# Performance work log

Measured on AMD Instinct MI355X. Metric: run time of the kernel, lower is better.

## Reference

```python
import jax, jax.numpy as jnp
import numpy as np

COMMITMENT = 0.25  # beta


def setup_inputs() -> dict:
    key = jax.random.key(0)
    k1, k2 = jax.random.split(key)
    B, M, D, K = 16, 4096, 64, 1024
    z_e = jax.random.normal(k1, (B, M, D), dtype=jnp.float32)
    embed = jax.random.normal(k2, (K, D), dtype=jnp.float32)  # codebook C in R^{KxD}
    return {"z_e": z_e, "embed": embed}


def reference(z_e, embed):
    """Eval-mode VQ forward: nearest-code lookup + VQ loss + straight-through.

    z_e:   (B, M, D) encoder outputs
    embed: (K, D) codebook
    Returns (z_q_st, indices, vq_loss).
    """
    B, M, D = z_e.shape
    flat = z_e.reshape(-1, D)  # (N, D)
    dist = (
        jnp.sum(flat * flat, axis=1, keepdims=True)
        - 2.0 * (flat @ embed.T)
        + jnp.sum(embed * embed, axis=1)[None, :]
    )
    indices = jnp.argmin(dist, axis=1)  # (N,)
    z_q = embed[indices].reshape(B, M, D)  # gather

    sg = jax.lax.stop_gradient
    codebook_loss = jnp.mean((z_q - sg(z_e)) ** 2)
    commitment_loss = jnp.mean((z_e - sg(z_q)) ** 2)
    vq_loss = codebook_loss + COMMITMENT * commitment_loss

    z_q_st = z_e + sg(z_q - z_e)  # straight-through estimator
    return z_q_st, indices.reshape(B, M), vq_loss
```

## Files before the change

kernel.cpp:

```cpp
#include <hip/hip_runtime.h>
#include <hip/hip_bf16.h>
#include <stdint.h>

#define D_     64
#define K_     1024
#define N_     65536
#define TPB    256
#define RPB    64
#define NBLK   (N_ / RPB)
#define MARGIN 0.06f

typedef __bf16 bf16x8 __attribute__((ext_vector_type(8)));
typedef float  f32x4  __attribute__((ext_vector_type(4)));

__device__ __forceinline__ unsigned short bf16_rne(float f) {
    union { float f; uint32_t u; } v; v.f = f;
    const uint32_t u = v.u;
    return (unsigned short)((u + 0x7fffu + ((u >> 16) & 1u)) >> 16);
}
__device__ __forceinline__ float bf16_tof(unsigned short h) {
    union { uint32_t u; float f; } v; v.u = ((uint32_t)h) << 16;
    return v.f;
}

__global__ __launch_bounds__(256) void vq_prep(const float* __restrict__ embed,
                                               double* __restrict__ n64,
                                               float* __restrict__ n32,
                                               char* __restrict__ eb) {
    const int gid = blockIdx.x * 256 + threadIdx.x;
    const int k   = gid >> 2;
    const int q4  = gid & 3;
    const float4* e4 = (const float4*)(embed + (size_t)k * D_ + q4 * 16);
    double acc = 0.0;
    uint32_t hw[8], lw[8];
#pragma unroll
    for (int q = 0; q < 4; ++q) {
        const float4 e = e4[q];
        float c[4] = {e.x, e.y, e.z, e.w};
        unsigned short hb[4], lb[4];
#pragma unroll
        for (int j = 0; j < 4; ++j) {
            hb[j] = bf16_rne(c[j]);
            lb[j] = bf16_rne(c[j] - bf16_tof(hb[j]));
            acc = fma((double)c[j], (double)c[j], acc);
        }
        hw[q * 2]     = (uint32_t)hb[0] | ((uint32_t)hb[1] << 16);
        hw[q * 2 + 1] = (uint32_t)hb[2] | ((uint32_t)hb[3] << 16);
        lw[q * 2]     = (uint32_t)lb[0] | ((uint32_t)lb[1] << 16);
        lw[q * 2 + 1] = (uint32_t)lb[2] | ((uint32_t)lb[3] << 16);
    }
    acc += __shfl_xor(acc, 1);
    acc += __shfl_xor(acc, 2);
    if (q4 == 0) { n64[k] = acc; n32[k] = (float)acc; }
    const int ct = k >> 4, cl = k & 15;
    char* hp = eb + (size_t)ct * 4096        + (q4 * 16 + cl) * 32;
    char* lp = eb + (size_t)ct * 4096 + 2048 + (q4 * 16 + cl) * 32;
    int4 h0; h0.x = hw[0]; h0.y = hw[1]; h0.z = hw[2]; h0.w = hw[3];
    int4 h1; h1.x = hw[4]; h1.y = hw[5]; h1.z = hw[6]; h1.w = hw[7];
    int4 l0; l0.x = lw[0]; l0.y = lw[1]; l0.z = lw[2]; l0.w = lw[3];
    int4 l1; l1.x = lw[4]; l1.y = lw[5]; l1.z = lw[6]; l1.w = lw[7];
    *(int4*)hp = h0; *(int4*)(hp + 16) = h1;
    *(int4*)lp = l0; *(int4*)(lp + 16) = l1;
}

__global__ __launch_bounds__(TPB) void vq_main(const float* __restrict__ z_e,
                                               const float* __restrict__ embed,
                                               const char* __restrict__ eb,
                                               const float* __restrict__ n32g,
                                               const double* __restrict__ n64g,
                                               float* __restrict__ out,
                                               float* __restrict__ partials) {
    __shared__ float red[TPB];

    const int tid  = threadIdx.x;
    const int lane = tid & 63;
    const int w    = tid >> 6;
    const int lg   = lane >> 4;
    const int lc   = lane & 15;
    const int wrow0 = blockIdx.x * RPB + w * 16;

    float  xs[16];
    bf16x8 ah[2], al[2];
    {
        const int row = wrow0 + lc;
        const float4* xg = (const float4*)(z_e + (size_t)row * D_ + lg * 16);
#pragma unroll
        for (int q = 0; q < 4; ++q) {
            const float4 x = xg[q];
            xs[q * 4 + 0] = x.x; xs[q * 4 + 1] = x.y;
            xs[q * 4 + 2] = x.z; xs[q * 4 + 3] = x.w;
        }
#pragma unroll
        for (int s = 0; s < 2; ++s) {
#pragma unroll
            for (int i = 0; i < 8; ++i) {
                const float xf = xs[s * 8 + i];
                const unsigned short hb = bf16_rne(xf);
                const unsigned short lb = bf16_rne(xf - bf16_tof(hb));
                union { unsigned short u; __bf16 h; } uh, ul;
                uh.u = hb; ul.u = lb;
                ah[s][i] = uh.h;
                al[s][i] = ul.h;
            }
        }
    }

    float b1[4], b2[4];
    int   i1[4];
#pragma unroll
    for (int rg = 0; rg < 4; ++rg) { b1[rg] = 3.4e38f; b2[rg] = 3.4e38f; i1[rg] = 0; }

    const char* ebl = eb + lane * 32;

#define LOADCT(CT, H0, H1, L0, L1, NV) {                                  \
        const char* p_ = ebl + (CT) * 4096;                               \
        H0 = *(const int4*)(p_);                                          \
        H1 = *(const int4*)(p_ + 16);                                     \
        L0 = *(const int4*)(p_ + 2048);                                   \
        L1 = *(const int4*)(p_ + 2064);                                   \
        NV = n32g[(CT) * 16 + lc];                                        \
    }
#define COMPUTECT(CT, H0, H1, L0, L1, NV) {                               \
        const bf16x8 bh0 = __builtin_bit_cast(bf16x8, H0);                \
        const bf16x8 bh1 = __builtin_bit_cast(bf16x8, H1);                \
        const bf16x8 bl0 = __builtin_bit_cast(bf16x8, L0);                \
        const bf16x8 bl1 = __builtin_bit_cast(bf16x8, L1);                \
        f32x4 acc0 = {0.f, 0.f, 0.f, 0.f};                                \
        f32x4 acc1 = {0.f, 0.f, 0.f, 0.f};                                \
        acc0 = __builtin_amdgcn_mfma_f32_16x16x32_bf16(ah[0], bh0, acc0, 0, 0, 0); \
        acc1 = __builtin_amdgcn_mfma_f32_16x16x32_bf16(ah[1], bh1, acc1, 0, 0, 0); \
        acc0 = __builtin_amdgcn_mfma_f32_16x16x32_bf16(al[0], bh0, acc0, 0, 0, 0); \
        acc1 = __builtin_amdgcn_mfma_f32_16x16x32_bf16(al[1], bh1, acc1, 0, 0, 0); \
        acc0 = __builtin_amdgcn_mfma_f32_16x16x32_bf16(ah[0], bl0, acc0, 0, 0, 0); \
        acc1 = __builtin_amdgcn_mfma_f32_16x16x32_bf16(ah[1], bl1, acc1, 0, 0, 0); \
        const int ki = (CT) * 16 + lc;                                    \
        _Pragma("unroll")                                                 \
        for (int rg = 0; rg < 4; ++rg) {                                  \
            const float s  = fmaf(-2.0f, acc0[rg] + acc1[rg], NV);        \
            const bool  lt = s < b1[rg];                                  \
            const float m2 = fminf(s, b2[rg]);                            \
            b2[rg] = lt ? b1[rg] : m2;                                    \
            b1[rg] = lt ? s      : b1[rg];                                \
            i1[rg] = lt ? ki     : i1[rg];                                \
        }                                                                 \
    }

    {
        int4 Ah0, Ah1, Al0, Al1; float Anv;
        int4 Bh0, Bh1, Bl0, Bl1; float Bnv;
        LOADCT(0, Ah0, Ah1, Al0, Al1, Anv);
        for (int ct = 0; ct < 64; ct += 2) {
            LOADCT(ct + 1, Bh0, Bh1, Bl0, Bl1, Bnv);
            COMPUTECT(ct, Ah0, Ah1, Al0, Al1, Anv);
            const int nct = (ct + 2 < 64) ? (ct + 2) : 0;
            LOADCT(nct, Ah0, Ah1, Al0, Al1, Anv);
            COMPUTECT(ct + 1, Bh0, Bh1, Bl0, Bl1, Bnv);
        }
    }
#undef LOADCT
#undef COMPUTECT

#pragma unroll
    for (int rg = 0; rg < 4; ++rg)
#pragma unroll
        for (int off = 1; off <= 8; off <<= 1) {
            const float ob1 = __shfl_xor(b1[rg], off);
            const float ob2 = __shfl_xor(b2[rg], off);
            const int   oi1 = __shfl_xor(i1[rg], off);
            if (ob1 < b1[rg] || (ob1 == b1[rg] && oi1 < i1[rg])) {
                b2[rg] = fminf(b1[rg], ob2); b1[rg] = ob1; i1[rg] = oi1;
            } else {
                b2[rg] = fminf(ob1, b2[rg]);
            }
        }

#pragma unroll
    for (int rg = 0; rg < 4; ++rg) {
        for (int g = 0; g < 4; ++g) {
            const float g1 = __shfl(b1[rg], g << 4);
            const float g2 = __shfl(b2[rg], g << 4);
            if (g2 - g1 < MARGIN) {
                const int grow = wrow0 + g * 4 + rg;
                const float* xp = z_e + (size_t)grow * D_;
                double bs = 1.0e300; int bi = 1 << 30;
                for (int c0 = 0; c0 < K_; c0 += 64) {
                    const int c = c0 + lane;
                    const float* ep = embed + (size_t)c * D_;
                    double dot = 0.0;
#pragma unroll
                    for (int j = 0; j < D_; ++j)
                        dot = fma((double)xp[j], (double)ep[j], dot);
                    const double sc = fma(-2.0, dot, n64g[c]);
                    if (sc < bs) { bs = sc; bi = c; }
                }
#pragma unroll
                for (int off = 32; off > 0; off >>= 1) {
                    const double so = __shfl_xor(bs, off);
                    const int    io = __shfl_xor(bi, off);
                    if (so < bs || (so == bs && io < bi)) { bs = so; bi = io; }
                }
                if (lg == g) i1[rg] = bi;
            }
        }
    }

    float sq = 0.f;
    {
        const int srcl = (lc >> 2) << 4;
        const int c0v = __shfl(i1[0], srcl);
        const int c1v = __shfl(i1[1], srcl);
        const int c2v = __shfl(i1[2], srcl);
        const int c3v = __shfl(i1[3], srcl);
        const int rsel = lc & 3;
        int bidx = (rsel == 0) ? c0v : (rsel == 1) ? c1v : (rsel == 2) ? c2v : c3v;
        bidx &= (K_ - 1);
        const int row = wrow0 + lc;
        const float4* eg = (const float4*)(embed + (size_t)bidx * D_ + lg * 16);
        float4*       og = (float4*)(out + (size_t)row * D_ + lg * 16);
#pragma unroll
        for (int q = 0; q < 4; ++q) {
            const float4 e = eg[q];
            const int   x0 = q * 4;
            const float d0 = e.x - xs[x0 + 0];
            const float d1 = e.y - xs[x0 + 1];
            const float d2 = e.z - xs[x0 + 2];
            const float d3 = e.w - xs[x0 + 3];
            sq = fmaf(d0, d0, sq); sq = fmaf(d1, d1, sq);
            sq = fmaf(d2, d2, sq); sq = fmaf(d3, d3, sq);
            float4 o;
            o.x = xs[x0 + 0] + d0;
            o.y = xs[x0 + 1] + d1;
            o.z = xs[x0 + 2] + d2;
            o.w = xs[x0 + 3] + d3;
            og[q] = o;
        }
        if (lg == 0) out[(size_t)N_ * D_ + row] = (float)bidx;
    }

    red[tid] = sq;
    __syncthreads();
#pragma unroll
    for (int s = TPB / 2; s > 0; s >>= 1) {
        if (tid < s) red[tid] += red[tid + s];
        __syncthreads();
    }
    if (tid == 0) partials[blockIdx.x] = red[0];
}

__global__ __launch_bounds__(256) void vq_loss_final(const float* __restrict__ partials,
                                                     float* __restrict__ out) {
    __shared__ float red[256];
    const int tid = threadIdx.x;
    float s = 0.f;
#pragma unroll
    for (int i = 0; i < NBLK / 256; ++i) s += partials[tid + i * 256];
    red[tid] = s;
    __syncthreads();
#pragma unroll
    for (int w = 128; w > 0; w >>= 1) {
        if (tid < w) red[tid] += red[tid + w];
        __syncthreads();
    }
    if (tid == 0)
        out[(size_t)N_ * D_ + N_] = 1.25f * red[0] / (float)((size_t)N_ * D_);
}

extern "C" void kernel_launch(void* const* d_in, const int* in_sizes, int n_in,
                              void* d_out, int out_size, void* d_ws, size_t ws_size,
                              hipStream_t stream) {
    const float* z_e;
    const float* embed;
    if (in_sizes[0] == N_ * D_) {
        z_e   = (const float*)d_in[0];
        embed = (const float*)d_in[1];
    } else {
        z_e   = (const float*)d_in[1];
        embed = (const float*)d_in[0];
    }
    float* out = (float*)d_out;

    double* n64      = (double*)d_ws;
    float*  n32      = (float*)(n64 + K_);
    float*  partials = n32 + K_;
    char*   eb       = (char*)(partials + NBLK);

    vq_prep<<<(K_ * 4) / 256, 256, 0, stream>>>(embed, n64, n32, eb);
    vq_main<<<NBLK, TPB, 0, stream>>>(z_e, embed, eb, n32, n64, out, partials);
    vq_loss_final<<<1, 256, 0, stream>>>(partials, out);
}
```

Measured before the change: 204.6 us.

## Use single-wave blocks, deeper codebook prefetch, and re-read inputs instead of holding registers

The main kernel now runs one 64-thread wave per block covering 16 rows, which removes the shared-memory block reduction and its barriers in favour of a wave shuffle reduction. The codebook loop loads two 16-code tiles per step with double buffering, deepening the prefetch. The fp32 input row is no longer kept in registers across the loop; it is re-read from global memory in the epilogue to lower register pressure. The prep kernel splits its double accumulation into two chains. In exchange there are four times as many blocks, vq_loss_final has more partials to sum, and the extra input read adds memory traffic.

```diff
diff --git a/kernel.cpp b/kernel.cpp
--- a/kernel.cpp
+++ b/kernel.cpp
@@ -5,8 +5,8 @@
 #define D_     64
 #define K_     1024
 #define N_     65536
-#define TPB    256
-#define RPB    64
+#define TPB    64
+#define RPB    16
 #define NBLK   (N_ / RPB)
 #define MARGIN 0.06f
 
@@ -23,15 +23,15 @@
     return v.f;
 }
 
-__global__ __launch_bounds__(256) void vq_prep(const float* __restrict__ embed,
-                                               double* __restrict__ n64,
-                                               float* __restrict__ n32,
-                                               char* __restrict__ eb) {
-    const int gid = blockIdx.x * 256 + threadIdx.x;
+__global__ __launch_bounds__(64) void vq_prep(const float* __restrict__ embed,
+                                              double* __restrict__ n64,
+                                              float* __restrict__ n32,
+                                              char* __restrict__ eb) {
+    const int gid = blockIdx.x * 64 + threadIdx.x;
     const int k   = gid >> 2;
     const int q4  = gid & 3;
     const float4* e4 = (const float4*)(embed + (size_t)k * D_ + q4 * 16);
-    double acc = 0.0;
+    double accA = 0.0, accB = 0.0;
     uint32_t hw[8], lw[8];
 #pragma unroll
     for (int q = 0; q < 4; ++q) {
@@ -42,13 +42,17 @@
         for (int j = 0; j < 4; ++j) {
             hb[j] = bf16_rne(c[j]);
             lb[j] = bf16_rne(c[j] - bf16_tof(hb[j]));
-            acc = fma((double)c[j], (double)c[j], acc);
-        }
+        }
+        accA = fma((double)c[0], (double)c[0], accA);
+        accB = fma((double)c[1], (double)c[1], accB);
+        accA = fma((double)c[2], (double)c[2], accA);
+        accB = fma((double)c[3], (double)c[3], accB);
         hw[q * 2]     = (uint32_t)hb[0] | ((uint32_t)hb[1] << 16);
         hw[q * 2 + 1] = (uint32_t)hb[2] | ((uint32_t)hb[3] << 16);
         lw[q * 2]     = (uint32_t)lb[0] | ((uint32_t)lb[1] << 16);
         lw[q * 2 + 1] = (uint32_t)lb[2] | ((uint32_t)lb[3] << 16);
     }
+    double acc = accA + accB;
     acc += __shfl_xor(acc, 1);
     acc += __shfl_xor(acc, 2);
     if (q4 == 0) { n64[k] = acc; n32[k] = (float)acc; }
@@ -70,20 +74,15 @@
                                                const double* __restrict__ n64g,
                                                float* __restrict__ out,
                                                float* __restrict__ partials) {
-    __shared__ float red[TPB];
-
-    const int tid  = threadIdx.x;
-    const int lane = tid & 63;
-    const int w    = tid >> 6;
+    const int lane = threadIdx.x;
     const int lg   = lane >> 4;
     const int lc   = lane & 15;
-    const int wrow0 = blockIdx.x * RPB + w * 16;
-
-    float  xs[16];
+    const int wrow0 = blockIdx.x * RPB;
+
     bf16x8 ah[2], al[2];
     {
-        const int row = wrow0 + lc;
-        const float4* xg = (const float4*)(z_e + (size_t)row * D_ + lg * 16);
+        const float4* xg = (const float4*)(z_e + (size_t)(wrow0 + lc) * D_ + lg * 16);
+        float xs[16];
 #pragma unroll
         for (int q = 0; q < 4; ++q) {
             const float4 x = xg[q];
@@ -112,15 +111,20 @@
 
     const char* ebl = eb + lane * 32;
 
-#define LOADCT(CT, H0, H1, L0, L1, NV) {                                  \
-        const char* p_ = ebl + (CT) * 4096;                               \
-        H0 = *(const int4*)(p_);                                          \
-        H1 = *(const int4*)(p_ + 16);                                     \
-        L0 = *(const int4*)(p_ + 2048);                                   \
-        L1 = *(const int4*)(p_ + 2064);                                   \
-        NV = n32g[(CT) * 16 + lc];                                        \
-    }
-#define COMPUTECT(CT, H0, H1, L0, L1, NV) {                               \
+#define LOADPAIR(P, R) {                                                  \
+        const char* p0_ = ebl + (size_t)(P) * 8192;                       \
+        R##h00 = *(const int4*)(p0_);                                     \
+        R##h01 = *(const int4*)(p0_ + 16);                                \
+        R##l00 = *(const int4*)(p0_ + 2048);                              \
+        R##l01 = *(const int4*)(p0_ + 2064);                              \
+        R##h10 = *(const int4*)(p0_ + 4096);                              \
+        R##h11 = *(const int4*)(p0_ + 4112);                              \
+        R##l10 = *(const int4*)(p0_ + 6144);                              \
+        R##l11 = *(const int4*)(p0_ + 6160);                              \
+        R##nv0 = n32g[(P) * 32 + lc];                                     \
+        R##nv1 = n32g[(P) * 32 + 16 + lc];                                \
+    }
+#define COMPGROUP(KI, H0, H1, L0, L1, NV) {                               \
         const bf16x8 bh0 = __builtin_bit_cast(bf16x8, H0);                \
         const bf16x8 bh1 = __builtin_bit_cast(bf16x8, H1);                \
         const bf16x8 bl0 = __builtin_bit_cast(bf16x8, L0);                \
@@ -133,7 +137,7 @@
         acc1 = __builtin_amdgcn_mfma_f32_16x16x32_bf16(al[1], bh1, acc1, 0, 0, 0); \
         acc0 = __builtin_amdgcn_mfma_f32_16x16x32_bf16(ah[0], bl0, acc0, 0, 0, 0); \
         acc1 = __builtin_amdgcn_mfma_f32_16x16x32_bf16(ah[1], bl1, acc1, 0, 0, 0); \
-        const int ki = (CT) * 16 + lc;                                    \
+        const int ki_ = (KI) + lc;                                        \
         _Pragma("unroll")                                                 \
         for (int rg = 0; rg < 4; ++rg) {                                  \
             const float s  = fmaf(-2.0f, acc0[rg] + acc1[rg], NV);        \
@@ -141,24 +145,29 @@
             const float m2 = fminf(s, b2[rg]);                            \
             b2[rg] = lt ? b1[rg] : m2;                                    \
             b1[rg] = lt ? s      : b1[rg];                                \
-            i1[rg] = lt ? ki     : i1[rg];                                \
+            i1[rg] = lt ? ki_    : i1[rg];                                \
         }                                                                 \
     }
+#define COMPPAIR(P, R) {                                                  \
+        COMPGROUP((P) * 32,      R##h00, R##h01, R##l00, R##l01, R##nv0); \
+        COMPGROUP((P) * 32 + 16, R##h10, R##h11, R##l10, R##l11, R##nv1); \
+    }
 
     {
-        int4 Ah0, Ah1, Al0, Al1; float Anv;
-        int4 Bh0, Bh1, Bl0, Bl1; float Bnv;
-        LOADCT(0, Ah0, Ah1, Al0, Al1, Anv);
-        for (int ct = 0; ct < 64; ct += 2) {
-            LOADCT(ct + 1, Bh0, Bh1, Bl0, Bl1, Bnv);
-            COMPUTECT(ct, Ah0, Ah1, Al0, Al1, Anv);
-            const int nct = (ct + 2 < 64) ? (ct + 2) : 0;
-            LOADCT(nct, Ah0, Ah1, Al0, Al1, Anv);
-            COMPUTECT(ct + 1, Bh0, Bh1, Bl0, Bl1, Bnv);
-        }
-    }
-#undef LOADCT
-#undef COMPUTECT
+        int4 Ah00, Ah01, Al00, Al01, Ah10, Ah11, Al10, Al11; float Anv0, Anv1;
+        int4 Bh00, Bh01, Bl00, Bl01, Bh10, Bh11, Bl10, Bl11; float Bnv0, Bnv1;
+        LOADPAIR(0, A);
+        for (int p = 0; p < 32; p += 2) {
+            LOADPAIR(p + 1, B);
+            COMPPAIR(p, A);
+            const int np = (p + 2 < 32) ? (p + 2) : 0;
+            LOADPAIR(np, A);
+            COMPPAIR(p + 1, B);
+        }
+    }
+#undef LOADPAIR
+#undef COMPGROUP
+#undef COMPPAIR
 
 #pragma unroll
     for (int rg = 0; rg < 4; ++rg)
@@ -216,35 +225,31 @@
         bidx &= (K_ - 1);
         const int row = wrow0 + lc;
         const float4* eg = (const float4*)(embed + (size_t)bidx * D_ + lg * 16);
+        const float4* xg = (const float4*)(z_e + (size_t)row * D_ + lg * 16);
         float4*       og = (float4*)(out + (size_t)row * D_ + lg * 16);
 #pragma unroll
         for (int q = 0; q < 4; ++q) {
             const float4 e = eg[q];
-            const int   x0 = q * 4;
-            const float d0 = e.x - xs[x0 + 0];
-            const float d1 = e.y - xs[x0 + 1];
-            const float d2 = e.z - xs[x0 + 2];
-            const float d3 = e.w - xs[x0 + 3];
+            const float4 x = xg[q];
+            const float d0 = e.x - x.x;
+            const float d1 = e.y - x.y;
+            const float d2 = e.z - x.z;
+            const float d3 = e.w - x.w;
             sq = fmaf(d0, d0, sq); sq = fmaf(d1, d1, sq);
             sq = fmaf(d2, d2, sq); sq = fmaf(d3, d3, sq);
             float4 o;
-            o.x = xs[x0 + 0] + d0;
-            o.y = xs[x0 + 1] + d1;
-            o.z = xs[x0 + 2] + d2;
-            o.w = xs[x0 + 3] + d3;
+            o.x = x.x + d0;
+            o.y = x.y + d1;
+            o.z = x.z + d2;
+            o.w = x.w + d3;
             og[q] = o;
         }
         if (lg == 0) out[(size_t)N_ * D_ + row] = (float)bidx;
     }
 
-    red[tid] = sq;
-    __syncthreads();
-#pragma unroll
-    for (int s = TPB / 2; s > 0; s >>= 1) {
-        if (tid < s) red[tid] += red[tid + s];
-        __syncthreads();
-    }
-    if (tid == 0) partials[blockIdx.x] = red[0];
+#pragma unroll
+    for (int off = 32; off > 0; off >>= 1) sq += __shfl_xor(sq, off);
+    if (lane == 0) partials[blockIdx.x] = sq;
 }
 
 __global__ __launch_bounds__(256) void vq_loss_final(const float* __restrict__ partials,
@@ -284,7 +289,7 @@
     float*  partials = n32 + K_;
     char*   eb       = (char*)(partials + NBLK);
 
-    vq_prep<<<(K_ * 4) / 256, 256, 0, stream>>>(embed, n64, n32, eb);
+    vq_prep<<<K_ / 16, 64, 0, stream>>>(embed, n64, n32, eb);
     vq_main<<<NBLK, TPB, 0, stream>>>(z_e, embed, eb, n32, n64, out, partials);
     vq_loss_final<<<1, 256, 0, stream>>>(partials, out);
 }
```

Result: faster. 193.5 us (-5.5%).
